# Performance work log

Hardware: AMD Instinct MI355X
Metric: run time of the kernel (lower is better)

The kernel has to match this reference:

```python
import jax, jax.numpy as jnp
import numpy as np

HEADS = 8
DIM_HEAD = 64
QUERY_DIM = 512
CONTEXT_DIM = 768
INNER_DIM = HEADS * DIM_HEAD  # 512
SCALE = DIM_HEAD ** -0.5


def setup_inputs() -> dict:
    key = jax.random.key(0)
    ks = jax.random.split(key, 7)
    B, N, M = 4, 2048, 1024
    x = jax.random.normal(ks[0], (B, N, QUERY_DIM), dtype=jnp.float32)
    context = jax.random.normal(ks[1], (B, M, CONTEXT_DIM), dtype=jnp.float32)
    # torch Linear weights stored as (out_features, in_features); y = x @ W.T
    Wq = jax.random.normal(ks[2], (INNER_DIM, QUERY_DIM), dtype=jnp.float32) * (QUERY_DIM ** -0.5)
    Wk = jax.random.normal(ks[3], (INNER_DIM, CONTEXT_DIM), dtype=jnp.float32) * (CONTEXT_DIM ** -0.5)
    Wv = jax.random.normal(ks[4], (INNER_DIM, CONTEXT_DIM), dtype=jnp.float32) * (CONTEXT_DIM ** -0.5)
    Wo = jax.random.normal(ks[5], (QUERY_DIM, INNER_DIM), dtype=jnp.float32) * (INNER_DIM ** -0.5)
    bo = jax.random.normal(ks[6], (QUERY_DIM,), dtype=jnp.float32) * 0.01
    return {"x": x, "context": context, "Wq": Wq, "Wk": Wk, "Wv": Wv, "Wo": Wo, "bo": bo}


def reference(x, context, Wq, Wk, Wv, Wo, bo):
    B, N, _ = x.shape
    M = context.shape[1]
    h, d = HEADS, DIM_HEAD
    q = jnp.einsum('bnc,ic->bni', x, Wq)        # [B,N,inner]
    k = jnp.einsum('bmc,ic->bmi', context, Wk)  # [B,M,inner]
    v = jnp.einsum('bmc,ic->bmi', context, Wv)  # [B,M,inner]
    # split heads: b n (h d) -> b h n d
    q = q.reshape(B, N, h, d).transpose(0, 2, 1, 3)
    k = k.reshape(B, M, h, d).transpose(0, 2, 1, 3)
    v = v.reshape(B, M, h, d).transpose(0, 2, 1, 3)
    # fp32 upcast for QK^T (inputs already fp32; kept explicit for fidelity)
    sim = jnp.einsum('bhnd,bhmd->bhnm', q.astype(jnp.float32), k.astype(jnp.float32)) * SCALE
    attn = jax.nn.softmax(sim, axis=-1)
    out = jnp.einsum('bhnm,bhmd->bhnd', attn, v)  # [B,h,N,d]
    out = out.transpose(0, 2, 1, 3).reshape(B, N, h * d)  # b n (h d)
    return jnp.einsum('bni,oi->bno', out, Wo) + bo  # dropout p=0 in eval
```

## Files before the change

kernel.cpp:

```cpp
#include <hip/hip_runtime.h>

using u16 = unsigned short;
typedef __bf16 bf16x8 __attribute__((ext_vector_type(8)));
typedef __bf16 bf16x2 __attribute__((ext_vector_type(2)));
typedef float  f32x4  __attribute__((ext_vector_type(4)));
typedef float  f32x16 __attribute__((ext_vector_type(16)));

#define MFMA16x16x32 __builtin_amdgcn_mfma_f32_16x16x32_bf16
#define MFMA32x32x16 __builtin_amdgcn_mfma_f32_32x32x16_bf16

#if __has_builtin(__builtin_amdgcn_exp2f)
#define EXP2 __builtin_amdgcn_exp2f
#else
#define EXP2 exp2f
#endif

static __device__ __forceinline__ unsigned f2bf_u(float f){
  unsigned x = __builtin_bit_cast(unsigned, f);
  return (x + 0x7fffu + ((x >> 16) & 1u)) >> 16;
}

static __device__ __forceinline__ void gll16(const void* g, void* l){
  __builtin_amdgcn_global_load_lds((const __attribute__((address_space(1))) void*)g,
                                   (__attribute__((address_space(3))) void*)l, 16, 0, 0);
}

static __device__ __forceinline__ f32x16 splat16(float x){
  f32x16 v;
#pragma unroll
  for (int i = 0; i < 16; ++i) v[i] = x;
  return v;
}

__global__ void __launch_bounds__(256) cvt_all(
    const float* __restrict__ x,  u16* __restrict__ xb,
    const float* __restrict__ cx, u16* __restrict__ cxb,
    const float* __restrict__ wq, u16* __restrict__ wqb,
    const float* __restrict__ wk, u16* __restrict__ wkb,
    const float* __restrict__ wv, u16* __restrict__ wvb,
    const float* __restrict__ wo, u16* __restrict__ wob)
{
  const float* in; u16* out; int n4;
  switch (blockIdx.y){
    case 0: in=x;  out=xb;  n4=(4*2048*512)/4; break;
    case 1: in=cx; out=cxb; n4=(4*1024*768)/4; break;
    case 2: in=wq; out=wqb; n4=(512*512)/4;    break;
    case 3: in=wk; out=wkb; n4=(512*768)/4;    break;
    case 4: in=wv; out=wvb; n4=(512*768)/4;    break;
    default:in=wo; out=wob; n4=(512*512)/4;    break;
  }
  int i = blockIdx.x*256 + threadIdx.x;
  const int stride = gridDim.x*256;
  for (; i < n4; i += stride){
    float4 f = ((const float4*)in)[i];
    ushort4 u;
    u.x = (u16)f2bf_u(f.x); u.y = (u16)f2bf_u(f.y);
    u.z = (u16)f2bf_u(f.z); u.w = (u16)f2bf_u(f.w);
    ((ushort4*)out)[i] = u;
  }
}

template<int LDA, int LDB, int KK, int OM>
static __device__ __forceinline__ void gemm_tile64(
    const u16* __restrict__ Ap, const u16* __restrict__ Bp,
    void* __restrict__ Cv, int ldc, int bx, int by,
    const float* __restrict__ bias, float scale,
    u16* __restrict__ sAp, u16* __restrict__ sBp)
{
  const int tid = threadIdx.x;
  const int w = tid >> 6, lane = tid & 63;
  const int wr = w >> 1, wc = w & 1;
  const long tm = (long)bx * 128;
  const long tn = (long)by * 64;

  f32x4 acc[4][2] = {};

  const int srl = lane >> 3, scc = lane & 7;

  auto stage = [&](int kt, int bb){
#pragma unroll
    for (int i = 0; i < 4; ++i){
      const int row = w*32 + i*8 + srl;
      const int sw = scc ^ (row & 7);
      gll16(Ap + (tm + row)*LDA + kt*64 + sw*8, sAp + bb*(128*64) + (w*32 + i*8)*64);
    }
#pragma unroll
    for (int i = 0; i < 2; ++i){
      const int row = w*16 + i*8 + srl;
      const int sw = scc ^ (row & 7);
      gll16(Bp + (tn + row)*LDB + kt*64 + sw*8, sBp + bb*(64*64) + (w*16 + i*8)*64);
    }
  };

  const int fr = lane & 15, fg = lane >> 4;
  constexpr int NK = KK / 64;

  stage(0, 0);
  __syncthreads();
  for (int kt = 0; kt < NK; ++kt){
    if (kt + 1 < NK) stage(kt + 1, (kt + 1) & 1);
    const int bb = kt & 1;
    bf16x8 af[4][2], bfr[2][2];
#pragma unroll
    for (int fm = 0; fm < 4; ++fm){
      const int row = wr*64 + fm*16 + fr;
      const int swz = row & 7;
#pragma unroll
      for (int s = 0; s < 2; ++s)
        af[fm][s] = *(const bf16x8*)&sAp[bb*(128*64) + row*64 + ((s*4 + fg) ^ swz)*8];
    }
#pragma unroll
    for (int fn = 0; fn < 2; ++fn){
      const int row = wc*32 + fn*16 + fr;
      const int swz = row & 7;
#pragma unroll
      for (int s = 0; s < 2; ++s)
        bfr[fn][s] = *(const bf16x8*)&sBp[bb*(64*64) + row*64 + ((s*4 + fg) ^ swz)*8];
    }
#pragma unroll
    for (int s = 0; s < 2; ++s)
#pragma unroll
      for (int fm = 0; fm < 4; ++fm)
#pragma unroll
        for (int fn = 0; fn < 2; ++fn)
          acc[fm][fn] = MFMA16x16x32(af[fm][s], bfr[fn][s], acc[fm][fn], 0, 0, 0);
    __syncthreads();
  }

#pragma unroll
  for (int fm = 0; fm < 4; ++fm){
#pragma unroll
    for (int fn = 0; fn < 2; ++fn){
      const long row0 = tm + wr*64 + fm*16 + fg*4;
      const long col  = tn + wc*32 + fn*16 + fr;
      if (OM == 0){
        u16* C = (u16*)Cv;
#pragma unroll
        for (int rr = 0; rr < 4; ++rr)
          C[(row0 + rr)*ldc + col] = (u16)f2bf_u(acc[fm][fn][rr] * scale);
      } else {
        float* C = (float*)Cv;
        const float bv = bias[col];
#pragma unroll
        for (int rr = 0; rr < 4; ++rr)
          C[(row0 + rr)*ldc + col] = acc[fm][fn][rr] + bv;
      }
    }
  }
}

template<int LDA, int LDB, int KK, int OM>
static __device__ __forceinline__ void gemm_tile128(
    const u16* __restrict__ Ap, const u16* __restrict__ Bp,
    void* __restrict__ Cv, int ldc, int bx, int by,
    const float* __restrict__ bias, float scale,
    u16* __restrict__ sAp, u16* __restrict__ sBp)
{
  const int tid = threadIdx.x;
  const int w = tid >> 6, lane = tid & 63;
  const int wr = w >> 1, wc = w & 1;
  const long tm = (long)bx * 128;
  const long tn = (long)by * 128;

  f32x4 acc[4][4] = {};

  const int srl = lane >> 3, scc = lane & 7;

  auto stage = [&](int kt, int bb){
#pragma unroll
    for (int i = 0; i < 4; ++i){
      const int row = w*32 + i*8 + srl;
      const int sw = scc ^ (row & 7);
      gll16(Ap + (tm + row)*LDA + kt*64 + sw*8, sAp + bb*(128*64) + (w*32 + i*8)*64);
      gll16(Bp + (tn + row)*LDB + kt*64 + sw*8, sBp + bb*(128*64) + (w*32 + i*8)*64);
    }
  };

  const int fr = lane & 15, fg = lane >> 4;
  constexpr int NK = KK / 64;

  stage(0, 0);
  __syncthreads();
  for (int kt = 0; kt < NK; ++kt){
    if (kt + 1 < NK) stage(kt + 1, (kt + 1) & 1);
    const int bb = kt & 1;
    bf16x8 af[4][2], bfr[4][2];
#pragma unroll
    for (int fm = 0; fm < 4; ++fm){
      const int row = wr*64 + fm*16 + fr;
      const int swz = row & 7;
#pragma unroll
      for (int s = 0; s < 2; ++s)
        af[fm][s] = *(const bf16x8*)&sAp[bb*(128*64) + row*64 + ((s*4 + fg) ^ swz)*8];
    }
#pragma unroll
    for (int fn = 0; fn < 4; ++fn){
      const int row = wc*64 + fn*16 + fr;
      const int swz = row & 7;
#pragma unroll
      for (int s = 0; s < 2; ++s)
        bfr[fn][s] = *(const bf16x8*)&sBp[bb*(128*64) + row*64 + ((s*4 + fg) ^ swz)*8];
    }
#pragma unroll
    for (int s = 0; s < 2; ++s)
#pragma unroll
      for (int fm = 0; fm < 4; ++fm)
#pragma unroll
        for (int fn = 0; fn < 4; ++fn)
          acc[fm][fn] = MFMA16x16x32(af[fm][s], bfr[fn][s], acc[fm][fn], 0, 0, 0);
    __syncthreads();
  }

#pragma unroll
  for (int fm = 0; fm < 4; ++fm){
#pragma unroll
    for (int fn = 0; fn < 4; ++fn){
      const long row0 = tm + wr*64 + fm*16 + fg*4;
      const long col  = tn + wc*64 + fn*16 + fr;
      if (OM == 0){
        u16* C = (u16*)Cv;
#pragma unroll
        for (int rr = 0; rr < 4; ++rr)
          C[(row0 + rr)*ldc + col] = (u16)f2bf_u(acc[fm][fn][rr] * scale);
      } else {
        float* C = (float*)Cv;
        const float bv = bias[col];
#pragma unroll
        for (int rr = 0; rr < 4; ++rr)
          C[(row0 + rr)*ldc + col] = acc[fm][fn][rr] + bv;
      }
    }
  }
}

__global__ __launch_bounds__(256, 2) void proj_fused(
    const u16* __restrict__ xb,  const u16* __restrict__ cxb,
    const u16* __restrict__ wqb, const u16* __restrict__ wkb,
    const u16* __restrict__ wvb,
    u16* __restrict__ qb, u16* __restrict__ kb, u16* __restrict__ vtb,
    float qscale)
{
  __shared__ u16 sA[2*128*64];
  __shared__ u16 sB[2*128*64];
  const int bid = blockIdx.x;
  const int lid = (bid & 7)*64 + (bid >> 3);
  if (lid < 256){
    gemm_tile128<512,512,512,0>(xb, wqb, (void*)qb, 512, lid >> 2, lid & 3,
                                nullptr, qscale, sA, sB);
  } else if (lid < 384){
    const int t = lid - 256;
    gemm_tile128<768,768,768,0>(cxb, wkb, (void*)kb, 512, t >> 2, t & 3,
                                nullptr, 1.0f, sA, sB);
  } else {
    const int t = lid - 384, z = t >> 5, r = t & 31;
    gemm_tile128<768,768,768,0>(wvb, cxb + (long)z*1024*768,
                                (void*)(vtb + (long)z*512*1024), 1024,
                                r >> 3, r & 7, nullptr, 1.0f, sA, sB);
  }
}

__global__ __launch_bounds__(256, 3) void gemm_out(
    const u16* __restrict__ ab, const u16* __restrict__ wob,
    float* __restrict__ out, const float* __restrict__ bias)
{
  __shared__ u16 sA[2*128*64];
  __shared__ u16 sB[2*64*64];
  const int bid = blockIdx.x;
  const int lid = (bid & 7)*64 + (bid >> 3);
  gemm_tile64<512,512,512,1>(ab, wob, (void*)out, 512, lid >> 3, lid & 7,
                             bias, 1.0f, sA, sB);
}

__global__ __launch_bounds__(256, 2) void attn_fwd(
    const u16* __restrict__ Q,
    const u16* __restrict__ Kb,
    const u16* __restrict__ Vt,
    u16* __restrict__ O)
{
  const int bid = blockIdx.x;
  const int lid = (bid & 7)*64 + (bid >> 3);
  const int qx = lid & 15, hh = (lid >> 4) & 7, b = lid >> 7;
  const int w = threadIdx.x >> 6, lane = threadIdx.x & 63;
  const int q31 = lane & 31, hi = lane >> 5;
  const int qw = w & 1, kvg = w >> 1;
  const int q0 = qx*128 + qw*64;

  __shared__ u16 sRing[8][64*64];
  __shared__ float sLsP[8*32];
  __shared__ float sLsT[4*32];

  bf16x8 qf[2][4];
#pragma unroll
  for (int j = 0; j < 2; ++j){
    const u16* qrow = Q + (long)(b*2048 + q0 + j*32 + q31)*512 + hh*64;
#pragma unroll
    for (int ks = 0; ks < 4; ++ks)
      qf[j][ks] = *(const bf16x8*)(qrow + ks*16 + hi*8);
  }

  f32x16 o[2][2] = {{splat16(0.f), splat16(0.f)}, {splat16(0.f), splat16(0.f)}};
  float lsum0 = 0.f, lsum1 = 0.f;

  const int srl = lane >> 3, scc = lane & 7;

  auto stagePair = [&](int u){
    const int tvs = 2*u + (w >> 1);
    const int sl = tvs & 3;
    if ((w & 1) == 0){
#pragma unroll
      for (int i = 0; i < 8; ++i){
        const int row = i*8 + srl;
        const int sw = scc ^ (row & 7);
        gll16(Kb + (long)(b*1024 + tvs*64 + row)*512 + hh*64 + sw*8,
              &sRing[sl][(i*8)*64]);
      }
    } else {
#pragma unroll
      for (int i = 0; i < 8; ++i){
        const int row = i*8 + srl;
        const int sw = scc ^ (row & 7);
        gll16(Vt + (long)(b*512 + hh*64 + row)*1024 + tvs*64 + sw*8,
              &sRing[4 + sl][(i*8)*64]);
      }
    }
  };

  stagePair(0);

  for (int t = 0; t < 8; ++t){
    asm volatile("s_waitcnt vmcnt(0)" ::: "memory");
    __builtin_amdgcn_s_barrier();
    asm volatile("" ::: "memory");
    if (t + 1 < 8) stagePair(t + 1);

    const int tv = 2*t + kvg;
    const int sl = tv & 3;
    const u16* sKp = sRing[sl];
    const u16* sVp = sRing[4 + sl];

#pragma unroll
    for (int mt = 0; mt < 2; ++mt){
      f32x16 s0 = splat16(-16.f), s1 = splat16(-16.f);
      const int row = mt*32 + q31;
      const int swz = row & 7;
      __builtin_amdgcn_s_setprio(1);
#pragma unroll
      for (int ks = 0; ks < 4; ++ks){
        bf16x8 kf = *(const bf16x8*)&sKp[row*64 + ((ks*2 + hi) ^ swz)*8];
        s0 = MFMA32x32x16(kf, qf[0][ks], s0, 0, 0, 0);
        s1 = MFMA32x32x16(kf, qf[1][ks], s1, 0, 0, 0);
      }
      __builtin_amdgcn_s_setprio(0);

      unsigned pk0[8], pk1[8];
#pragma unroll
      for (int r = 0; r < 16; ++r){ s0[r] = EXP2(s0[r]); lsum0 += s0[r]; }
#pragma unroll
      for (int r = 0; r < 16; ++r){ s1[r] = EXP2(s1[r]); lsum1 += s1[r]; }
#pragma unroll
      for (int p2 = 0; p2 < 8; ++p2){
        union { bf16x2 h; unsigned u; } t0, t1;
        t0.h[0] = (__bf16)s0[2*p2]; t0.h[1] = (__bf16)s0[2*p2 + 1]; pk0[p2] = t0.u;
        t1.h[0] = (__bf16)s1[2*p2]; t1.h[1] = (__bf16)s1[2*p2 + 1]; pk1[p2] = t1.u;
      }

#pragma unroll
      for (int sl2 = 0; sl2 < 2; ++sl2){
        union { unsigned u[4]; bf16x8 v; } pa0, pa1;
        {
          const unsigned ca = pk0[sl2*4 + 0], cb = pk0[sl2*4 + 1];
          const unsigned cc = pk0[sl2*4 + 2], cd = pk0[sl2*4 + 3];
          const unsigned ya = hi ? ca : cc;
          const unsigned za = (unsigned)__shfl_xor((int)ya, 32);
          const unsigned yb = hi ? cb : cd;
          const unsigned zb = (unsigned)__shfl_xor((int)yb, 32);
          pa0.u[0] = hi ? za : ca;
          pa0.u[1] = hi ? zb : cb;
          pa0.u[2] = hi ? cc : za;
          pa0.u[3] = hi ? cd : zb;
        }
        {
          const unsigned ca = pk1[sl2*4 + 0], cb = pk1[sl2*4 + 1];
          const unsigned cc = pk1[sl2*4 + 2], cd = pk1[sl2*4 + 3];
          const unsigned ya = hi ? ca : cc;
          const unsigned za = (unsigned)__shfl_xor((int)ya, 32);
          const unsigned yb = hi ? cb : cd;
          const unsigned zb = (unsigned)__shfl_xor((int)yb, 32);
          pa1.u[0] = hi ? za : ca;
          pa1.u[1] = hi ? zb : cb;
          pa1.u[2] = hi ? cc : za;
          pa1.u[3] = hi ? cd : zb;
        }
        const int s = mt*2 + sl2;
        __builtin_amdgcn_s_setprio(1);
#pragma unroll
        for (int fd = 0; fd < 2; ++fd){
          const int vrow = fd*32 + q31;
          bf16x8 bv = *(const bf16x8*)&sVp[vrow*64 + (((s*2 + hi) ^ (vrow & 7)))*8];
          o[0][fd] = MFMA32x32x16(pa0.v, bv, o[0][fd], 0, 0, 0);
          o[1][fd] = MFMA32x32x16(pa1.v, bv, o[1][fd], 0, 0, 0);
        }
        __builtin_amdgcn_s_setprio(0);
      }
    }
    asm volatile("" ::: "memory");
  }

  lsum0 += __shfl_xor(lsum0, 32);
  lsum1 += __shfl_xor(lsum1, 32);
  sLsP[(w*2 + 0)*32 + q31] = lsum0;
  sLsP[(w*2 + 1)*32 + q31] = lsum1;
  __syncthreads();

  float* sO = (float*)&sRing[0][0];
  if (kvg == 1){
#pragma unroll
    for (int j = 0; j < 2; ++j){
#pragma unroll
      for (int fd = 0; fd < 2; ++fd){
        float* p = sO + (((qw*2 + j)*2 + fd)*64*20) + lane*20;
#pragma unroll
        for (int k = 0; k < 4; ++k){
          f32x4 t4;
#pragma unroll
          for (int e = 0; e < 4; ++e) t4[e] = o[j][fd][4*k + e];
          *(f32x4*)(p + 4*k) = t4;
        }
      }
    }
  }
  __syncthreads();

  if (kvg == 0){
#pragma unroll
    for (int j = 0; j < 2; ++j){
#pragma unroll
      for (int fd = 0; fd < 2; ++fd){
        const float* p = sO + (((qw*2 + j)*2 + fd)*64*20) + lane*20;
#pragma unroll
        for (int k = 0; k < 4; ++k){
          f32x4 t4 = *(const f32x4*)(p + 4*k);
#pragma unroll
          for (int e = 0; e < 4; ++e) o[j][fd][4*k + e] += t4[e];
        }
      }
    }
    const float lt0 = lsum0 + sLsP[((2 + qw)*2 + 0)*32 + q31];
    const float lt1 = lsum1 + sLsP[((2 + qw)*2 + 1)*32 + q31];
    sLsT[(qw*2 + 0)*32 + q31] = lt0;
    sLsT[(qw*2 + 1)*32 + q31] = lt1;
  }
  __syncthreads();

  if (kvg == 0){
#pragma unroll
    for (int j = 0; j < 2; ++j){
      f32x4 inv[4];
#pragma unroll
      for (int g = 0; g < 4; ++g){
        f32x4 ls = *(const f32x4*)&sLsT[(qw*2 + j)*32 + 8*g + 4*hi];
#pragma unroll
        for (int e = 0; e < 4; ++e) inv[g][e] = 1.0f / ls[e];
      }
      u16* orow = O + (long)(b*2048 + q0 + j*32)*512 + hh*64;
#pragma unroll
      for (int fd = 0; fd < 2; ++fd){
#pragma unroll
        for (int r = 0; r < 16; ++r){
          const int q = (r & 3) + 8*(r >> 2) + 4*hi;
          const float val = o[j][fd][r] * inv[r >> 2][r & 3];
          orow[(long)q*512 + fd*32 + q31] = (u16)f2bf_u(val);
        }
      }
    }
  }
}

extern "C" void kernel_launch(void* const* d_in, const int* in_sizes, int n_in,
                              void* d_out, int out_size, void* d_ws, size_t ws_size,
                              hipStream_t stream)
{
  (void)in_sizes; (void)n_in; (void)out_size; (void)ws_size;
  const float* x   = (const float*)d_in[0];
  const float* ctx = (const float*)d_in[1];
  const float* Wq  = (const float*)d_in[2];
  const float* Wk  = (const float*)d_in[3];
  const float* Wv  = (const float*)d_in[4];
  const float* Wo  = (const float*)d_in[5];
  const float* bo  = (const float*)d_in[6];
  float* out = (float*)d_out;

  char* ws = (char*)d_ws;
  u16* xb  = (u16*)(ws + 0);
  u16* cxb = (u16*)(ws + 8388608);
  u16* wqb = (u16*)(ws + 14680064);
  u16* wkb = (u16*)(ws + 15204352);
  u16* wvb = (u16*)(ws + 15990784);
  u16* wob = (u16*)(ws + 16777216);
  u16* qb  = (u16*)(ws + 17301504);
  u16* kb  = (u16*)(ws + 25690112);
  u16* vtb = (u16*)(ws + 29884416);
  u16* ab  = (u16*)(ws + 34078720);

  cvt_all<<<dim3(1024, 6, 1), 256, 0, stream>>>(x, xb, ctx, cxb, Wq, wqb,
                                                Wk, wkb, Wv, wvb, Wo, wob);

  proj_fused<<<dim3(512, 1, 1), 256, 0, stream>>>(
      xb, cxb, wqb, wkb, wvb, qb, kb, vtb, 0.18033688011112042f);

  attn_fwd<<<dim3(512, 1, 1), 256, 0, stream>>>(qb, kb, vtb, ab);

  gemm_out<<<dim3(512, 1, 1), 256, 0, stream>>>(ab, wob, out, bo);
}
```

Baseline: 69.27 us.

## Split attention KV sequence across four wave groups with 512-thread blocks

Doubles the attention block to 512 threads (8 waves). Each block now splits the KV sequence into four groups of 32-row tiles, double-buffered, instead of two groups of 64-row tiles. Staging uses a deeper prefetch with a partial vmcnt wait, and V tiles get a new 32-column swizzle. Partial outputs and row sums are reduced across the four groups in two LDS tree stages. This is meant to raise parallelism and latency hiding, at the cost of extra barriers, more reduction work, and higher LDS and register pressure per block.

```diff
diff --git a/kernel.cpp b/kernel.cpp
--- a/kernel.cpp
+++ b/kernel.cpp
@@ -31,6 +31,8 @@
   for (int i = 0; i < 16; ++i) v[i] = x;
   return v;
 }
+
+static __device__ __forceinline__ int vswz(int r){ return (r ^ (r >> 2)) & 3; }
 
 __global__ void __launch_bounds__(256) cvt_all(
     const float* __restrict__ x,  u16* __restrict__ xb,
@@ -271,7 +273,7 @@
                              bias, 1.0f, sA, sB);
 }
 
-__global__ __launch_bounds__(256, 2) void attn_fwd(
+__global__ __launch_bounds__(512, 4) void attn_fwd(
     const u16* __restrict__ Q,
     const u16* __restrict__ Kb,
     const u16* __restrict__ Vt,
@@ -282,11 +284,11 @@
   const int qx = lid & 15, hh = (lid >> 4) & 7, b = lid >> 7;
   const int w = threadIdx.x >> 6, lane = threadIdx.x & 63;
   const int q31 = lane & 31, hi = lane >> 5;
-  const int qw = w & 1, kvg = w >> 1;
+  const int qw = w >> 2, g = w & 3;
   const int q0 = qx*128 + qw*64;
 
-  __shared__ u16 sRing[8][64*64];
-  __shared__ float sLsP[8*32];
+  __shared__ u16 sBuf[2][8][2048];
+  __shared__ float sLsP[16*32];
   __shared__ float sLsT[4*32];
 
   bf16x8 qf[2][4];
@@ -302,46 +304,46 @@
   float lsum0 = 0.f, lsum1 = 0.f;
 
   const int srl = lane >> 3, scc = lane & 7;
-
-  auto stagePair = [&](int u){
-    const int tvs = 2*u + (w >> 1);
-    const int sl = tvs & 3;
-    if ((w & 1) == 0){
-#pragma unroll
-      for (int i = 0; i < 8; ++i){
+  const int vrl = lane >> 2, vcc = lane & 3;
+
+  auto stage = [&](int u){
+    const int tv = g*8 + u;
+    const int bb = u & 1;
+    if (qw == 0){
+#pragma unroll
+      for (int i = 0; i < 4; ++i){
         const int row = i*8 + srl;
-        const int sw = scc ^ (row & 7);
-        gll16(Kb + (long)(b*1024 + tvs*64 + row)*512 + hh*64 + sw*8,
-              &sRing[sl][(i*8)*64]);
+        const int cs = scc ^ (row & 7);
+        gll16(Kb + (long)(b*1024 + tv*32 + row)*512 + hh*64 + cs*8,
+              &sBuf[bb][g][(i*8)*64]);
       }
     } else {
 #pragma unroll
-      for (int i = 0; i < 8; ++i){
-        const int row = i*8 + srl;
-        const int sw = scc ^ (row & 7);
-        gll16(Vt + (long)(b*512 + hh*64 + row)*1024 + tvs*64 + sw*8,
-              &sRing[4 + sl][(i*8)*64]);
+      for (int i = 0; i < 4; ++i){
+        const int row = i*16 + vrl;
+        const int cs = vcc ^ vswz(row);
+        gll16(Vt + (long)(b*512 + hh*64 + row)*1024 + tv*32 + cs*8,
+              &sBuf[bb][4 + g][(i*16)*32]);
       }
     }
   };
 
-  stagePair(0);
-
-  for (int t = 0; t < 8; ++t){
-    asm volatile("s_waitcnt vmcnt(0)" ::: "memory");
+  stage(0);
+  stage(1);
+
+  for (int u = 0; u < 8; ++u){
+    if (u < 7) asm volatile("s_waitcnt vmcnt(4)" ::: "memory");
+    else       asm volatile("s_waitcnt vmcnt(0)" ::: "memory");
     __builtin_amdgcn_s_barrier();
     asm volatile("" ::: "memory");
-    if (t + 1 < 8) stagePair(t + 1);
-
-    const int tv = 2*t + kvg;
-    const int sl = tv & 3;
-    const u16* sKp = sRing[sl];
-    const u16* sVp = sRing[4 + sl];
-
-#pragma unroll
-    for (int mt = 0; mt < 2; ++mt){
-      f32x16 s0 = splat16(-16.f), s1 = splat16(-16.f);
-      const int row = mt*32 + q31;
+
+    const int bb = u & 1;
+    const u16* sKp = sBuf[bb][g];
+    const u16* sVp = sBuf[bb][4 + g];
+
+    f32x16 s0 = splat16(-16.f), s1 = splat16(-16.f);
+    {
+      const int row = q31;
       const int swz = row & 7;
       __builtin_amdgcn_s_setprio(1);
 #pragma unroll
@@ -351,59 +353,62 @@
         s1 = MFMA32x32x16(kf, qf[1][ks], s1, 0, 0, 0);
       }
       __builtin_amdgcn_s_setprio(0);
-
-      unsigned pk0[8], pk1[8];
-#pragma unroll
-      for (int r = 0; r < 16; ++r){ s0[r] = EXP2(s0[r]); lsum0 += s0[r]; }
-#pragma unroll
-      for (int r = 0; r < 16; ++r){ s1[r] = EXP2(s1[r]); lsum1 += s1[r]; }
-#pragma unroll
-      for (int p2 = 0; p2 < 8; ++p2){
-        union { bf16x2 h; unsigned u; } t0, t1;
-        t0.h[0] = (__bf16)s0[2*p2]; t0.h[1] = (__bf16)s0[2*p2 + 1]; pk0[p2] = t0.u;
-        t1.h[0] = (__bf16)s1[2*p2]; t1.h[1] = (__bf16)s1[2*p2 + 1]; pk1[p2] = t1.u;
-      }
-
-#pragma unroll
-      for (int sl2 = 0; sl2 < 2; ++sl2){
-        union { unsigned u[4]; bf16x8 v; } pa0, pa1;
-        {
-          const unsigned ca = pk0[sl2*4 + 0], cb = pk0[sl2*4 + 1];
-          const unsigned cc = pk0[sl2*4 + 2], cd = pk0[sl2*4 + 3];
-          const unsigned ya = hi ? ca : cc;
-          const unsigned za = (unsigned)__shfl_xor((int)ya, 32);
-          const unsigned yb = hi ? cb : cd;
-          const unsigned zb = (unsigned)__shfl_xor((int)yb, 32);
-          pa0.u[0] = hi ? za : ca;
-          pa0.u[1] = hi ? zb : cb;
-          pa0.u[2] = hi ? cc : za;
-          pa0.u[3] = hi ? cd : zb;
-        }
-        {
-          const unsigned ca = pk1[sl2*4 + 0], cb = pk1[sl2*4 + 1];
-          const unsigned cc = pk1[sl2*4 + 2], cd = pk1[sl2*4 + 3];
-          const unsigned ya = hi ? ca : cc;
-          const unsigned za = (unsigned)__shfl_xor((int)ya, 32);
-          const unsigned yb = hi ? cb : cd;
-          const unsigned zb = (unsigned)__shfl_xor((int)yb, 32);
-          pa1.u[0] = hi ? za : ca;
-          pa1.u[1] = hi ? zb : cb;
-          pa1.u[2] = hi ? cc : za;
-          pa1.u[3] = hi ? cd : zb;
-        }
-        const int s = mt*2 + sl2;
-        __builtin_amdgcn_s_setprio(1);
-#pragma unroll
-        for (int fd = 0; fd < 2; ++fd){
-          const int vrow = fd*32 + q31;
-          bf16x8 bv = *(const bf16x8*)&sVp[vrow*64 + (((s*2 + hi) ^ (vrow & 7)))*8];
-          o[0][fd] = MFMA32x32x16(pa0.v, bv, o[0][fd], 0, 0, 0);
-          o[1][fd] = MFMA32x32x16(pa1.v, bv, o[1][fd], 0, 0, 0);
-        }
-        __builtin_amdgcn_s_setprio(0);
-      }
-    }
+    }
+
+    unsigned pk0[8], pk1[8];
+#pragma unroll
+    for (int r = 0; r < 16; ++r){ s0[r] = EXP2(s0[r]); lsum0 += s0[r]; }
+#pragma unroll
+    for (int r = 0; r < 16; ++r){ s1[r] = EXP2(s1[r]); lsum1 += s1[r]; }
+#pragma unroll
+    for (int p2 = 0; p2 < 8; ++p2){
+      union { bf16x2 h; unsigned u; } t0, t1;
+      t0.h[0] = (__bf16)s0[2*p2]; t0.h[1] = (__bf16)s0[2*p2 + 1]; pk0[p2] = t0.u;
+      t1.h[0] = (__bf16)s1[2*p2]; t1.h[1] = (__bf16)s1[2*p2 + 1]; pk1[p2] = t1.u;
+    }
+
+#pragma unroll
+    for (int sl2 = 0; sl2 < 2; ++sl2){
+      union { unsigned u[4]; bf16x8 v; } pa0, pa1;
+      {
+        const unsigned ca = pk0[sl2*4 + 0], cb = pk0[sl2*4 + 1];
+        const unsigned cc = pk0[sl2*4 + 2], cd = pk0[sl2*4 + 3];
+        const unsigned ya = hi ? ca : cc;
+        const unsigned za = (unsigned)__shfl_xor((int)ya, 32);
+        const unsigned yb = hi ? cb : cd;
+        const unsigned zb = (unsigned)__shfl_xor((int)yb, 32);
+        pa0.u[0] = hi ? za : ca;
+        pa0.u[1] = hi ? zb : cb;
+        pa0.u[2] = hi ? cc : za;
+        pa0.u[3] = hi ? cd : zb;
+      }
+      {
+        const unsigned ca = pk1[sl2*4 + 0], cb = pk1[sl2*4 + 1];
+        const unsigned cc = pk1[sl2*4 + 2], cd = pk1[sl2*4 + 3];
+        const unsigned ya = hi ? ca : cc;
+        const unsigned za = (unsigned)__shfl_xor((int)ya, 32);
+        const unsigned yb = hi ? cb : cd;
+        const unsigned zb = (unsigned)__shfl_xor((int)yb, 32);
+        pa1.u[0] = hi ? za : ca;
+        pa1.u[1] = hi ? zb : cb;
+        pa1.u[2] = hi ? cc : za;
+        pa1.u[3] = hi ? cd : zb;
+      }
+      __builtin_amdgcn_s_setprio(1);
+#pragma unroll
+      for (int fd = 0; fd < 2; ++fd){
+        const int vrow = fd*32 + q31;
+        bf16x8 bv = *(const bf16x8*)&sVp[vrow*32 + (((sl2*2 + hi) ^ vswz(vrow)))*8];
+        o[0][fd] = MFMA32x32x16(pa0.v, bv, o[0][fd], 0, 0, 0);
+        o[1][fd] = MFMA32x32x16(pa1.v, bv, o[1][fd], 0, 0, 0);
+      }
+      __builtin_amdgcn_s_setprio(0);
+    }
+
     asm volatile("" ::: "memory");
+    __builtin_amdgcn_s_barrier();
+    asm volatile("" ::: "memory");
+    if (u + 2 < 8) stage(u + 2);
   }
 
   lsum0 += __shfl_xor(lsum0, 32);
@@ -412,55 +417,91 @@
   sLsP[(w*2 + 1)*32 + q31] = lsum1;
   __syncthreads();
 
-  float* sO = (float*)&sRing[0][0];
-  if (kvg == 1){
+  float* sO = (float*)&sBuf[0][0][0];
+  {
+    const int base = (((qw*2 + 0)*2 + 0)*64 + lane)*16;
+    if (g == 1 || g == 3){
+      float* R = sO + (g == 3 ? 8192 : 0);
+#pragma unroll
+      for (int j = 0; j < 2; ++j)
+#pragma unroll
+        for (int fd = 0; fd < 2; ++fd){
+          float* p = R + base + (j*2 + fd)*64*16;
+#pragma unroll
+          for (int k = 0; k < 4; ++k){
+            f32x4 t4;
+#pragma unroll
+            for (int e = 0; e < 4; ++e) t4[e] = o[j][fd][4*k + e];
+            *(f32x4*)(p + 4*k) = t4;
+          }
+        }
+    }
+    __syncthreads();
+    if (g == 0 || g == 2){
+      const float* R = sO + (g == 2 ? 8192 : 0);
+#pragma unroll
+      for (int j = 0; j < 2; ++j)
+#pragma unroll
+        for (int fd = 0; fd < 2; ++fd){
+          const float* p = R + base + (j*2 + fd)*64*16;
+#pragma unroll
+          for (int k = 0; k < 4; ++k){
+            f32x4 t4 = *(const f32x4*)(p + 4*k);
+#pragma unroll
+            for (int e = 0; e < 4; ++e) o[j][fd][4*k + e] += t4[e];
+          }
+        }
+    }
+    __syncthreads();
+    if (g == 2){
+#pragma unroll
+      for (int j = 0; j < 2; ++j)
+#pragma unroll
+        for (int fd = 0; fd < 2; ++fd){
+          float* p = sO + base + (j*2 + fd)*64*16;
+#pragma unroll
+          for (int k = 0; k < 4; ++k){
+            f32x4 t4;
+#pragma unroll
+            for (int e = 0; e < 4; ++e) t4[e] = o[j][fd][4*k + e];
+            *(f32x4*)(p + 4*k) = t4;
+          }
+        }
+    }
+    __syncthreads();
+    if (g == 0){
+#pragma unroll
+      for (int j = 0; j < 2; ++j)
+#pragma unroll
+        for (int fd = 0; fd < 2; ++fd){
+          const float* p = sO + base + (j*2 + fd)*64*16;
+#pragma unroll
+          for (int k = 0; k < 4; ++k){
+            f32x4 t4 = *(const f32x4*)(p + 4*k);
+#pragma unroll
+            for (int e = 0; e < 4; ++e) o[j][fd][4*k + e] += t4[e];
+          }
+        }
+    }
+  }
+
+  if (g == 0){
 #pragma unroll
     for (int j = 0; j < 2; ++j){
-#pragma unroll
-      for (int fd = 0; fd < 2; ++fd){
-        float* p = sO + (((qw*2 + j)*2 + fd)*64*20) + lane*20;
-#pragma unroll
-        for (int k = 0; k < 4; ++k){
-          f32x4 t4;
-#pragma unroll
-          for (int e = 0; e < 4; ++e) t4[e] = o[j][fd][4*k + e];
-          *(f32x4*)(p + 4*k) = t4;
-        }
-      }
-    }
-  }
-  __syncthreads();
-
-  if (kvg == 0){
-#pragma unroll
-    for (int j = 0; j < 2; ++j){
-#pragma unroll
-      for (int fd = 0; fd < 2; ++fd){
-        const float* p = sO + (((qw*2 + j)*2 + fd)*64*20) + lane*20;
-#pragma unroll
-        for (int k = 0; k < 4; ++k){
-          f32x4 t4 = *(const f32x4*)(p + 4*k);
-#pragma unroll
-          for (int e = 0; e < 4; ++e) o[j][fd][4*k + e] += t4[e];
-        }
-      }
-    }
-    const float lt0 = lsum0 + sLsP[((2 + qw)*2 + 0)*32 + q31];
-    const float lt1 = lsum1 + sLsP[((2 + qw)*2 + 1)*32 + q31];
-    sLsT[(qw*2 + 0)*32 + q31] = lt0;
-    sLsT[(qw*2 + 1)*32 + q31] = lt1;
-  }
-  __syncthreads();
-
-  if (kvg == 0){
+      float lt = 0.f;
+#pragma unroll
+      for (int gg = 0; gg < 4; ++gg)
+        lt += sLsP[((qw*4 + gg)*2 + j)*32 + q31];
+      sLsT[(qw*2 + j)*32 + q31] = lt;
+    }
 #pragma unroll
     for (int j = 0; j < 2; ++j){
       f32x4 inv[4];
 #pragma unroll
-      for (int g = 0; g < 4; ++g){
-        f32x4 ls = *(const f32x4*)&sLsT[(qw*2 + j)*32 + 8*g + 4*hi];
-#pragma unroll
-        for (int e = 0; e < 4; ++e) inv[g][e] = 1.0f / ls[e];
+      for (int gq = 0; gq < 4; ++gq){
+        f32x4 ls = *(const f32x4*)&sLsT[(qw*2 + j)*32 + 8*gq + 4*hi];
+#pragma unroll
+        for (int e = 0; e < 4; ++e) inv[gq][e] = 1.0f / ls[e];
       }
       u16* orow = O + (long)(b*2048 + q0 + j*32)*512 + hh*64;
 #pragma unroll
@@ -508,7 +549,7 @@
   proj_fused<<<dim3(512, 1, 1), 256, 0, stream>>>(
       xb, cxb, wqb, wkb, wvb, qb, kb, vtb, 0.18033688011112042f);
 
-  attn_fwd<<<dim3(512, 1, 1), 256, 0, stream>>>(qb, kb, vtb, ab);
+  attn_fwd<<<dim3(512, 1, 1), 512, 0, stream>>>(qb, kb, vtb, ab);
 
   gemm_out<<<dim3(512, 1, 1), 256, 0, stream>>>(ab, wob, out, bo);
 }
```

New measurement: 211.0 us. +204.7%, slower.
